# Kernel tuning notes

Measured on AMD Instinct MI355X. Metric: run time of the kernel, lower is better.

Reference implementation:

```python
import jax, jax.numpy as jnp
import numpy as np

CUTOFF = 5.0
NLINKED = 1
CELL_LIST = CUTOFF / NLINKED  # linked-cell edge length
_r = np.arange(-NLINKED, NLINKED + 1)
# torch.cartesian_prod(r1,r1,r1) == meshgrid(indexing='ij') stacked & flattened
LINKED = np.stack(np.meshgrid(_r, _r, _r, indexing='ij'), axis=-1).reshape(1, -1, 3).astype(np.float32)  # (1, 27, 3)


def setup_inputs() -> dict:
    N = 2744
    L = 30.0
    key = jax.random.key(0)
    k1, k2 = jax.random.split(key)
    coordinates = jax.random.uniform(k1, (N, 3), dtype=jnp.float32) * L
    cell = jnp.eye(3, dtype=jnp.float32) * L
    mass = jax.random.uniform(k2, (N,), dtype=jnp.float32) * 15.0 + 1.0
    period_table = jnp.ones((3,), dtype=jnp.int32)  # fully periodic
    return {"period_table": period_table, "coordinates": coordinates, "cell": cell, "mass": mass}


def _forward(period_table, coordinates, cell, mass):
    numatom = coordinates.shape[0]
    # wrap coordinates into the cell relative to atom 0 (fractional coords)
    inv_cell = jnp.linalg.inv(cell)
    inv_coor = coordinates @ inv_cell
    inv_coor = inv_coor - jnp.round(inv_coor - inv_coor[0])
    coordinates = inv_coor @ cell
    # remove center of mass
    com = (mass @ coordinates) / jnp.sum(mass)
    coordinates = coordinates - com[None, :]
    # periodic replicas needed to cover the cutoff
    num_repeats = jnp.ceil(jnp.min(CUTOFF / jnp.abs(cell), axis=0)).astype(jnp.int32)
    num_repeats = period_table.astype(jnp.int32) * num_repeats
    up = num_repeats + 1
    down = -num_repeats
    rs = [jnp.arange(int(down[i]), int(up[i])) for i in range(3)]
    g = jnp.meshgrid(*rs, indexing='ij')
    shifts_frac = jnp.stack(g, axis=-1).reshape(-1, 3).astype(coordinates.dtype)  # (S, 3)
    shifts = shifts_frac @ cell  # (S, 3) cartesian shift vectors
    num_shifts = shifts.shape[0]
    # prod = cartesian_prod(all_shifts, all_atoms).T : row0 shift idx, row1 atom idx
    prod0 = jnp.repeat(jnp.arange(num_shifts), numatom)
    prod1 = jnp.tile(jnp.arange(numatom), num_shifts)
    # shift box so all coords are positive; pad by cutoff
    mincoor = jnp.min(coordinates, axis=0) - CUTOFF - 1e-6
    coordinates = coordinates - mincoor
    maxcoor = jnp.max(coordinates, axis=0) + CUTOFF
    # all periodic images, keep only those inside the padded box
    image = (coordinates[None, :, :] + shifts[:, None, :]).reshape(-1, 3)
    keep = jnp.nonzero(((image < maxcoor) & (image > 0)).all(axis=1))[0]
    image_mask = image[keep]                      # (M, 3)
    prod0 = prod0[keep]
    prod1 = prod1[keep]
    # linked-cell indices
    ori_image_index = jnp.floor(coordinates / CELL_LIST)         # (N, 3)
    neigh_cell = ori_image_index[:, None, :] + jnp.asarray(LINKED)  # (N, 27, 3)
    image_index = jnp.floor(image_mask / CELL_LIST)              # (M, 3)
    max_cell_index = jnp.ceil(maxcoor / CELL_LIST)
    f10 = max_cell_index[1] * max_cell_index[0]
    neigh_cell_index = neigh_cell[:, :, 2] * f10 + neigh_cell[:, :, 1] * max_cell_index[0] + neigh_cell[:, :, 0]  # (N, 27)
    nimage_index = image_index[:, 2] * f10 + image_index[:, 1] * max_cell_index[0] + image_index[:, 0]            # (M,)
    # dense (N, M, 27) cell-index equality -- the memory-bound hot spot
    eq = neigh_cell_index[:, None, :] == nimage_index[None, :, None]
    ai, aj, _ = jnp.nonzero(eq)
    # distance filter on candidate pairs
    d = jnp.linalg.norm(coordinates[ai] - image_mask[aj], axis=-1)
    pair = jnp.nonzero((d < CUTOFF) & (d > 0.001))[0]
    center = ai[pair]
    img = aj[pair]
    shift_idx = prod0[img]
    atom_j = prod1[img]
    neigh_list = jnp.stack([center, atom_j])  # (2, P)
    return neigh_list, shifts[shift_idx], shifts_frac, shift_idx


def reference(period_table, coordinates, cell, mass):
    neigh_list, shifts_out, _, _ = _forward(period_table, coordinates, cell, mass)
    return (neigh_list, shifts_out)
```

## Files before the change

### kernel.cpp

```cpp
#include <hip/hip_runtime.h>
#include <math.h>

#define S_CAP  27
#define MAXNB  128
#define CUT    5.0f
#define NTHR   256
#define GRP    64
#define NMAX   2744



__device__ __forceinline__ void load_cell(const float* __restrict__ cell, float c[3][3])
{
    #pragma unroll
    for (int i = 0; i < 3; i++)
        #pragma unroll
        for (int j = 0; j < 3; j++) c[i][j] = cell[3 * i + j];
}

__device__ __forceinline__ void header_and_shifts(
    const float c[3][3], const int* __restrict__ period,
    const double* __restrict__ pd, const float* __restrict__ pf, int nblkA,
    float* sF, int* sI, float* s_shifts)
{
    #pragma clang fp contract(off)
    int t = threadIdx.x;
    if (t < 64) {
        double SM = 0.0, SX = 0.0, SY = 0.0, SZ = 0.0;
        float MN0 =  __builtin_inff(), MN1 =  __builtin_inff(), MN2 =  __builtin_inff();
        float MX0 = -__builtin_inff(), MX1 = -__builtin_inff(), MX2 = -__builtin_inff();
        for (int b = t; b < nblkA; b += 64) {
            SM += pd[4*b+0]; SX += pd[4*b+1]; SY += pd[4*b+2]; SZ += pd[4*b+3];
            MN0 = fminf(MN0, pf[6*b+0]); MN1 = fminf(MN1, pf[6*b+1]); MN2 = fminf(MN2, pf[6*b+2]);
            MX0 = fmaxf(MX0, pf[6*b+3]); MX1 = fmaxf(MX1, pf[6*b+4]); MX2 = fmaxf(MX2, pf[6*b+5]);
        }
        #pragma unroll
        for (int off = 32; off > 0; off >>= 1) {
            SM += __shfl_down(SM, off, 64);
            SX += __shfl_down(SX, off, 64);
            SY += __shfl_down(SY, off, 64);
            SZ += __shfl_down(SZ, off, 64);
            MN0 = fminf(MN0, __shfl_down(MN0, off, 64));
            MN1 = fminf(MN1, __shfl_down(MN1, off, 64));
            MN2 = fminf(MN2, __shfl_down(MN2, off, 64));
            MX0 = fmaxf(MX0, __shfl_down(MX0, off, 64));
            MX1 = fmaxf(MX1, __shfl_down(MX1, off, 64));
            MX2 = fmaxf(MX2, __shfl_down(MX2, off, 64));
        }
        if (t == 0) {
            float den  = (float)SM;
            float com0 = ((float)SX) / den;
            float com1 = ((float)SY) / den;
            float com2 = ((float)SZ) / den;
            float m20 = ((MN0 - com0) - CUT) - 1e-6f;
            float m21 = ((MN1 - com1) - CUT) - 1e-6f;
            float m22 = ((MN2 - com2) - CUT) - 1e-6f;
            float maxc0 = ((MX0 - com0) - m20) + CUT;
            float maxc1 = ((MX1 - com1) - m21) + CUT;
            float maxc2 = ((MX2 - com2) - m22) + CUT;
            float mcell0 = ceilf(maxc0 / CUT);
            float mcell1 = ceilf(maxc1 / CUT);
            float f10 = mcell1 * mcell0;
            int nr[3];
            for (int j = 0; j < 3; j++) {
                float v = __builtin_inff();
                for (int i = 0; i < 3; i++) {
                    float q = CUT / fabsf(c[i][j]);
                    v = fminf(v, q);
                }
                nr[j] = (int)ceilf(v);
                nr[j] *= period[j];
            }
            int nsz0 = 2*nr[0]+1, nsz1 = 2*nr[1]+1, nsz2 = 2*nr[2]+1;
            int S = nsz0 * nsz1 * nsz2;
            if (S > S_CAP) S = S_CAP;
            sI[0] = S;
            sI[1] = -nr[0]; sI[2] = -nr[1]; sI[3] = -nr[2];
            sI[4] = nsz1;   sI[5] = nsz2;
            sI[6] = (int)mcell0;
            sI[7] = (int)f10;
            sF[0] = maxc0; sF[1] = maxc1; sF[2] = maxc2;
            sF[3] = f10;   sF[4] = mcell0;
            sF[5] = m20;   sF[6] = m21;   sF[7] = m22;
            sF[8] = com0;  sF[9] = com1;  sF[10] = com2;
        }
    }
    __syncthreads();
    int S = sI[0];
    if (t < S) {
        int n1 = sI[4], n2 = sI[5];
        int i0 = t / (n1 * n2);
        int rem = t - i0 * n1 * n2;
        int i1 = rem / n2;
        int i2 = rem - i1 * n2;
        float fx = (float)(sI[1] + i0);
        float fy = (float)(sI[2] + i1);
        float fz = (float)(sI[3] + i2);
        #pragma unroll
        for (int d = 0; d < 3; d++)
            s_shifts[3*t + d] = fx*c[0][d] + fy*c[1][d] + fz*c[2][d];
    }
    __syncthreads();
}

__global__ __launch_bounds__(NTHR)
void kA_wrap(const float* __restrict__ coor, const float* __restrict__ cell,
             const float* __restrict__ mass, float* __restrict__ xv,
             int* __restrict__ sc_agg,
             int* __restrict__ grp_sum, int* __restrict__ grp_arrive,
             double* __restrict__ pd, float* __restrict__ pf, int n, int nagg, int ng)
{
    #pragma clang fp contract(off)
    __shared__ double wsum[4][4];
    __shared__ float  wred[4][6];
    int t    = threadIdx.x;
    int bid  = blockIdx.x;
    int gtid = bid * NTHR + t;
    int lane = t & 63;
    int w    = t >> 6;

    if (gtid < nagg) sc_agg[gtid] = -1;
    if (gtid < ng)   { grp_sum[gtid] = -1; grp_arrive[gtid] = 0; }

    float c[3][3];
    load_cell(cell, c);
    float a00 = c[1][1]*c[2][2] - c[1][2]*c[2][1];
    float a01 = c[0][2]*c[2][1] - c[0][1]*c[2][2];
    float a02 = c[0][1]*c[1][2] - c[0][2]*c[1][1];
    float a10 = c[1][2]*c[2][0] - c[1][0]*c[2][2];
    float a11 = c[0][0]*c[2][2] - c[0][2]*c[2][0];
    float a12 = c[0][2]*c[1][0] - c[0][0]*c[1][2];
    float a20 = c[1][0]*c[2][1] - c[1][1]*c[2][0];
    float a21 = c[0][1]*c[2][0] - c[0][0]*c[2][1];
    float a22 = c[0][0]*c[1][1] - c[0][1]*c[1][0];
    float det = c[0][0]*a00 + c[0][1]*a10 + c[0][2]*a20;
    float inv[3][3] = {{a00/det, a01/det, a02/det},
                       {a10/det, a11/det, a12/det},
                       {a20/det, a21/det, a22/det}};
    float f0[3];
    #pragma unroll
    for (int d = 0; d < 3; d++)
        f0[d] = coor[0]*inv[0][d] + coor[1]*inv[1][d] + coor[2]*inv[2][d];

    double sm = 0.0, sx = 0.0, sy = 0.0, sz = 0.0;
    float mn0 =  __builtin_inff(), mn1 =  __builtin_inff(), mn2 =  __builtin_inff();
    float mx0 = -__builtin_inff(), mx1 = -__builtin_inff(), mx2 = -__builtin_inff();
    if (gtid < n) {
        float p0 = coor[3*gtid], p1 = coor[3*gtid+1], p2 = coor[3*gtid+2];
        float ic[3], ww[3], x[3];
        #pragma unroll
        for (int d = 0; d < 3; d++)
            ic[d] = p0*inv[0][d] + p1*inv[1][d] + p2*inv[2][d];
        #pragma unroll
        for (int d = 0; d < 3; d++)
            ww[d] = ic[d] - rintf(ic[d] - f0[d]);
        #pragma unroll
        for (int d = 0; d < 3; d++)
            x[d] = ww[0]*c[0][d] + ww[1]*c[1][d] + ww[2]*c[2][d];
        xv[3*gtid] = x[0]; xv[3*gtid+1] = x[1]; xv[3*gtid+2] = x[2];
        float m = mass[gtid];
        sm = (double)m;
        sx = (double)m * (double)x[0];
        sy = (double)m * (double)x[1];
        sz = (double)m * (double)x[2];
        mn0 = x[0]; mn1 = x[1]; mn2 = x[2];
        mx0 = x[0]; mx1 = x[1]; mx2 = x[2];
    }
    #pragma unroll
    for (int off = 32; off > 0; off >>= 1) {
        sm += __shfl_down(sm, off, 64);
        sx += __shfl_down(sx, off, 64);
        sy += __shfl_down(sy, off, 64);
        sz += __shfl_down(sz, off, 64);
        mn0 = fminf(mn0, __shfl_down(mn0, off, 64));
        mn1 = fminf(mn1, __shfl_down(mn1, off, 64));
        mn2 = fminf(mn2, __shfl_down(mn2, off, 64));
        mx0 = fmaxf(mx0, __shfl_down(mx0, off, 64));
        mx1 = fmaxf(mx1, __shfl_down(mx1, off, 64));
        mx2 = fmaxf(mx2, __shfl_down(mx2, off, 64));
    }
    if (lane == 0) {
        wsum[w][0] = sm; wsum[w][1] = sx; wsum[w][2] = sy; wsum[w][3] = sz;
        wred[w][0] = mn0; wred[w][1] = mn1; wred[w][2] = mn2;
        wred[w][3] = mx0; wred[w][4] = mx1; wred[w][5] = mx2;
    }
    __syncthreads();
    if (t == 0) {
        double SM = 0.0, SX = 0.0, SY = 0.0, SZ = 0.0;
        float MN0 =  __builtin_inff(), MN1 =  __builtin_inff(), MN2 =  __builtin_inff();
        float MX0 = -__builtin_inff(), MX1 = -__builtin_inff(), MX2 = -__builtin_inff();
        #pragma unroll
        for (int q = 0; q < 4; q++) {
            SM += wsum[q][0]; SX += wsum[q][1]; SY += wsum[q][2]; SZ += wsum[q][3];
            MN0 = fminf(MN0, wred[q][0]); MN1 = fminf(MN1, wred[q][1]); MN2 = fminf(MN2, wred[q][2]);
            MX0 = fmaxf(MX0, wred[q][3]); MX1 = fmaxf(MX1, wred[q][4]); MX2 = fmaxf(MX2, wred[q][5]);
        }
        pd[bid*4+0] = SM; pd[bid*4+1] = SX; pd[bid*4+2] = SY; pd[bid*4+3] = SZ;
        pf[bid*6+0] = MN0; pf[bid*6+1] = MN1; pf[bid*6+2] = MN2;
        pf[bid*6+3] = MX0; pf[bid*6+4] = MX1; pf[bid*6+5] = MX2;
    }
}

__global__ __launch_bounds__(NTHR, 4)
void kC_search_emit(const int* __restrict__ period, const float* __restrict__ cell,
                    const double* __restrict__ pd, const float* __restrict__ pf,
                    const float* __restrict__ xv,
                    int* __restrict__ sc_agg, int* __restrict__ grp_sum,
                    int* __restrict__ grp_arrive,
                    float* __restrict__ out, int nblkA, int nblkC, int n, int P)
{
    #pragma clang fp contract(off)
    __shared__ float sF[12];
    __shared__ int   sI[8];
    __shared__ float s_shifts[3 * S_CAP];
    __shared__ float sux[NMAX], suy[NMAX], suz[NMAX];
    __shared__ int   lst[4][MAXNB];
    __shared__ int   s_np[4];
    __shared__ int   sExcl;
    __shared__ int   sFin;

    const int t    = threadIdx.x;
    const int bid  = blockIdx.x;
    const int lane = t & 63;
    const int w    = t >> 6;
    const int g    = bid / GRP;
    const int gpos = bid - g * GRP;
    const int gbase = g * GRP;
    const int gsz  = min(GRP, nblkC - gbase);

    if (n > NMAX) return;

    float c[3][3];
    load_cell(cell, c);
    header_and_shifts(c, period, pd, pf, nblkA, sF, sI, s_shifts);

    float a00 = c[1][1]*c[2][2] - c[1][2]*c[2][1];
    float a01 = c[0][2]*c[2][1] - c[0][1]*c[2][2];
    float a02 = c[0][1]*c[1][2] - c[0][2]*c[1][1];
    float a10 = c[1][2]*c[2][0] - c[1][0]*c[2][2];
    float a11 = c[0][0]*c[2][2] - c[0][2]*c[2][0];
    float a12 = c[0][2]*c[1][0] - c[0][0]*c[1][2];
    float a20 = c[1][0]*c[2][1] - c[1][1]*c[2][0];
    float a21 = c[0][1]*c[2][0] - c[0][0]*c[2][1];
    float a22 = c[0][0]*c[1][1] - c[0][1]*c[1][0];
    float det = c[0][0]*a00 + c[0][1]*a10 + c[0][2]*a20;
    float inv[3][3] = {{a00/det, a01/det, a02/det},
                       {a10/det, a11/det, a12/det},
                       {a20/det, a21/det, a22/det}};

    {
        const float m20 = sF[5], m21 = sF[6], m22 = sF[7];
        const float com0 = sF[8], com1 = sF[9], com2 = sF[10];
        for (int j = t; j < n; j += NTHR) {
            sux[j] = (xv[3*j]   - com0) - m20;
            suy[j] = (xv[3*j+1] - com1) - m21;
            suz[j] = (xv[3*j+2] - com2) - m22;
        }
    }
    __syncthreads();

    const int atom = bid * 4 + w;
    const bool valid = atom < n;

    {
        int cnt = 0;
        if (valid) {
            const float xi = sux[atom], yi = suy[atom], zi = suz[atom];
            const int d0 = sI[1], d1 = sI[2], d2 = sI[3];
            const int nsz1 = sI[4], nsz2 = sI[5];
            for (int jb = 0; jb < n; jb += 64) {
                int j = jb + lane;
                bool ok = false; int gg = 0;
                if (j < n) {
                    float ujx = sux[j], ujy = suy[j], ujz = suz[j];
                    float dx = xi - ujx, dy = yi - ujy, dz = zi - ujz;
                    float fr0 = rintf(dx*inv[0][0] + dy*inv[1][0] + dz*inv[2][0]);
                    float fr1 = rintf(dx*inv[0][1] + dy*inv[1][1] + dz*inv[2][1]);
                    float fr2 = rintf(dx*inv[0][2] + dy*inv[1][2] + dz*inv[2][2]);
                    float sx = fr0*c[0][0] + fr1*c[1][0] + fr2*c[2][0];
                    float sy = fr0*c[0][1] + fr1*c[1][1] + fr2*c[2][1];
                    float sz = fr0*c[0][2] + fr1*c[1][2] + fr2*c[2][2];
                    float imx = ujx + sx, imy = ujy + sy, imz = ujz + sz;
                    float ddx = xi - imx, ddy = yi - imy, ddz = zi - imz;
                    float ss = ddx*ddx + ddy*ddy + ddz*ddz;
                    float dd = sqrtf(ss);
                    ok = (dd < CUT) && (dd > 0.001f);
                    int i0 = (int)fr0 - d0, i1 = (int)fr1 - d1, i2 = (int)fr2 - d2;
                    int idx = (i0 * nsz1 + i1) * nsz2 + i2;
                    gg = idx * n + j;
                }
                unsigned long long m = __ballot(ok);
                int posn = cnt + (int)__popcll(m & ((1ull << lane) - 1ull));
                if (ok && posn < MAXNB) lst[w][posn] = gg;
                cnt += (int)__popcll(m);
            }
            if (cnt > MAXNB) cnt = MAXNB;
        }
        if (lane == 0) s_np[w] = cnt;
    }
    __syncthreads();

    if (t == 0) {
        int agg = s_np[0] + s_np[1] + s_np[2] + s_np[3];
        __hip_atomic_store(&sc_agg[bid], agg, __ATOMIC_RELAXED, __HIP_MEMORY_SCOPE_AGENT);
        int r = __hip_atomic_fetch_add(&grp_arrive[g], 1, __ATOMIC_ACQ_REL, __HIP_MEMORY_SCOPE_AGENT);
        sFin = (r == gsz - 1) ? 1 : 0;
    }
    __syncthreads();

    if (sFin && w == 0) {
        int idx = gbase + lane;
        int v = 0;
        if (lane < gsz)
            v = __hip_atomic_load(&sc_agg[idx], __ATOMIC_RELAXED, __HIP_MEMORY_SCOPE_AGENT);
        #pragma unroll
        for (int off = 32; off > 0; off >>= 1)
            v += __shfl_down(v, off, 64);
        if (lane == 0)
            __hip_atomic_store(&grp_sum[g], v, __ATOMIC_RELAXED, __HIP_MEMORY_SCOPE_AGENT);
    }

    if (w == 0) {
        int v1 = 0;
        if (lane < g) {
            v1 = __hip_atomic_load(&grp_sum[lane], __ATOMIC_RELAXED, __HIP_MEMORY_SCOPE_AGENT);
            while (v1 == -1) {
                __builtin_amdgcn_s_sleep(2);
                v1 = __hip_atomic_load(&grp_sum[lane], __ATOMIC_RELAXED, __HIP_MEMORY_SCOPE_AGENT);
            }
        }
        int v2 = 0;
        if (lane < gpos) {
            int idx = gbase + lane;
            v2 = __hip_atomic_load(&sc_agg[idx], __ATOMIC_RELAXED, __HIP_MEMORY_SCOPE_AGENT);
            while (v2 == -1) {
                __builtin_amdgcn_s_sleep(2);
                v2 = __hip_atomic_load(&sc_agg[idx], __ATOMIC_RELAXED, __HIP_MEMORY_SCOPE_AGENT);
            }
        }
        int v = v1 + v2;
        #pragma unroll
        for (int off = 32; off > 0; off >>= 1)
            v += __shfl_down(v, off, 64);
        if (lane == 0) sExcl = v;
    }
    __syncthreads();

    if (valid) {
        int cnt = s_np[w];
        int base = sExcl;
        for (int q = 0; q < w; q++) base += s_np[q];
        for (int r = lane; r < cnt; r += 64) {
            int gg = lst[w][r];
            int rank = 0;
            for (int q = 0; q < cnt; q++) rank += (lst[w][q] < gg) ? 1 : 0;
            int p = base + rank;
            if (p < P) {
                int sidx = gg / n;
                int a = gg - sidx * n;
                out[p]     = (float)atom;
                out[P + p] = (float)a;
                out[2*P + 3*p]     = s_shifts[3*sidx];
                out[2*P + 3*p + 1] = s_shifts[3*sidx + 1];
                out[2*P + 3*p + 2] = s_shifts[3*sidx + 2];
            }
        }
    }
}

extern "C" void kernel_launch(void* const* d_in, const int* in_sizes, int n_in,
                              void* d_out, int out_size, void* d_ws, size_t ws_size,
                              hipStream_t stream)
{
    const int*   period = (const int*)d_in[0];
    const float* coor   = (const float*)d_in[1];
    const float* cell   = (const float*)d_in[2];
    const float* mass   = (const float*)d_in[3];
    float* out = (float*)d_out;

    int n = in_sizes[1] / 3;
    int P = out_size / 5;

    char* wp = (char*)d_ws;
    size_t off = 0;
    auto alloc = [&](size_t bytes) -> void* {
        off = (off + 15) & ~(size_t)15;
        void* pp = (void*)(wp + off); off += bytes; return pp;
    };

    int nblkA = (n + NTHR - 1) / NTHR;
    int nblkC = (n + 3) / 4;
    int ng    = (nblkC + GRP - 1) / GRP;

    float*  xv       = (float*) alloc(3 * (size_t)n * 4);
    double* pd       = (double*)alloc((size_t)nblkA * 4 * 8);
    float*  pf       = (float*) alloc((size_t)nblkA * 6 * 4);
    int*    sc_agg   = (int*)   alloc((size_t)nblkC * 4);
    int*    grp_sum  = (int*)   alloc((size_t)ng * 4);
    int*    grp_arr  = (int*)   alloc((size_t)ng * 4);
    (void)ws_size; (void)n_in;

    hipLaunchKernelGGL(kA_wrap, dim3(nblkA), dim3(NTHR), 0, stream,
                       coor, cell, mass, xv, sc_agg, grp_sum, grp_arr,
                       pd, pf, n, nblkC, ng);
    hipLaunchKernelGGL(kC_search_emit, dim3(nblkC), dim3(NTHR), 0, stream,
                       period, cell, pd, pf, xv,
                       sc_agg, grp_sum, grp_arr, out, nblkA, nblkC, n, P);
}
```

Measured before the change: 96.47 us.

## Fuse wrap kernel into search kernel with spin-waited partial reductions

Merges the coordinate-wrapping kernel into the neighbor-search kernel. Each block recomputes all wrapped coordinates straight into shared memory, and the first NSEG blocks also publish per-segment COM and min/max partials. All blocks spin on sentinel values, set by a memset to 0xFF, until those partials are ready. This removes one kernel launch and the global xv round trip, at the cost of redundant per-block wrap work. It adds an inter-block dependency that assumes the producer blocks are resident, and the grp_arrive counter now starts at -1 via memset, which explains the gsz-2 change.

```diff
diff --git a/kernel.cpp b/kernel.cpp
--- a/kernel.cpp
+++ b/kernel.cpp
@@ -7,7 +7,7 @@
 #define NTHR   256
 #define GRP    64
 #define NMAX   2744
-
+#define NSEG   11
 
 
 __device__ __forceinline__ void load_cell(const float* __restrict__ cell, float c[3][3])
@@ -18,21 +18,169 @@
         for (int j = 0; j < 3; j++) c[i][j] = cell[3 * i + j];
 }
 
-__device__ __forceinline__ void header_and_shifts(
-    const float c[3][3], const int* __restrict__ period,
-    const double* __restrict__ pd, const float* __restrict__ pf, int nblkA,
-    float* sF, int* sI, float* s_shifts)
+__global__ __launch_bounds__(NTHR, 4)
+void k_fused(const int* __restrict__ period, const float* __restrict__ coor,
+             const float* __restrict__ cell, const float* __restrict__ mass,
+             double* __restrict__ pd, float* __restrict__ pf,
+             int* __restrict__ sc_agg, int* __restrict__ grp_sum,
+             int* __restrict__ grp_arrive,
+             float* __restrict__ out, int nblkA, int nblkC, int n, int P)
 {
     #pragma clang fp contract(off)
-    int t = threadIdx.x;
+    __shared__ float  sux[NMAX], suy[NMAX], suz[NMAX];
+    __shared__ double wsum[4][4];
+    __shared__ float  wred[4][6];
+    __shared__ float  sF[12];
+    __shared__ int    sI[8];
+    __shared__ float  s_shifts[3 * S_CAP];
+    __shared__ int    lst[4][MAXNB];
+    __shared__ int    s_np[4];
+    __shared__ int    sExcl;
+    __shared__ int    sFin;
+
+    const int t    = threadIdx.x;
+    const int bid  = blockIdx.x;
+    const int lane = t & 63;
+    const int w    = t >> 6;
+    const int g    = bid / GRP;
+    const int gpos = bid - g * GRP;
+    const int gbase = g * GRP;
+    const int gsz  = min(GRP, nblkC - gbase);
+
+    if (n > NMAX) return;
+
+    float c[3][3];
+    load_cell(cell, c);
+    float a00 = c[1][1]*c[2][2] - c[1][2]*c[2][1];
+    float a01 = c[0][2]*c[2][1] - c[0][1]*c[2][2];
+    float a02 = c[0][1]*c[1][2] - c[0][2]*c[1][1];
+    float a10 = c[1][2]*c[2][0] - c[1][0]*c[2][2];
+    float a11 = c[0][0]*c[2][2] - c[0][2]*c[2][0];
+    float a12 = c[0][2]*c[1][0] - c[0][0]*c[1][2];
+    float a20 = c[1][0]*c[2][1] - c[1][1]*c[2][0];
+    float a21 = c[0][1]*c[2][0] - c[0][0]*c[2][1];
+    float a22 = c[0][0]*c[1][1] - c[0][1]*c[1][0];
+    float det = c[0][0]*a00 + c[0][1]*a10 + c[0][2]*a20;
+    float inv[3][3] = {{a00/det, a01/det, a02/det},
+                       {a10/det, a11/det, a12/det},
+                       {a20/det, a21/det, a22/det}};
+    float f0[3];
+    #pragma unroll
+    for (int d = 0; d < 3; d++)
+        f0[d] = coor[0]*inv[0][d] + coor[1]*inv[1][d] + coor[2]*inv[2][d];
+
+    const bool producer = bid < nblkA;
+
+    for (int k = 0; k < NSEG; k++) {
+        int seg = producer ? (k == 0 ? bid : (k <= bid ? k - 1 : k)) : k;
+        int a = seg * NTHR + t;
+        bool va = a < n;
+        float x0 = 0.0f, x1 = 0.0f, x2 = 0.0f;
+        if (va) {
+            float p0 = coor[3*a], p1 = coor[3*a+1], p2 = coor[3*a+2];
+            float ic[3], ww[3];
+            #pragma unroll
+            for (int d = 0; d < 3; d++)
+                ic[d] = p0*inv[0][d] + p1*inv[1][d] + p2*inv[2][d];
+            #pragma unroll
+            for (int d = 0; d < 3; d++)
+                ww[d] = ic[d] - rintf(ic[d] - f0[d]);
+            x0 = ww[0]*c[0][0] + ww[1]*c[1][0] + ww[2]*c[2][0];
+            x1 = ww[0]*c[0][1] + ww[1]*c[1][1] + ww[2]*c[2][1];
+            x2 = ww[0]*c[0][2] + ww[1]*c[1][2] + ww[2]*c[2][2];
+            sux[a] = x0; suy[a] = x1; suz[a] = x2;
+        }
+        if (producer && k == 0) {
+            double sm = 0.0, sx = 0.0, sy = 0.0, sz = 0.0;
+            float mn0 =  __builtin_inff(), mn1 =  __builtin_inff(), mn2 =  __builtin_inff();
+            float mx0 = -__builtin_inff(), mx1 = -__builtin_inff(), mx2 = -__builtin_inff();
+            if (va) {
+                float m = mass[a];
+                sm = (double)m;
+                sx = (double)m * (double)x0;
+                sy = (double)m * (double)x1;
+                sz = (double)m * (double)x2;
+                mn0 = x0; mn1 = x1; mn2 = x2;
+                mx0 = x0; mx1 = x1; mx2 = x2;
+            }
+            #pragma unroll
+            for (int off = 32; off > 0; off >>= 1) {
+                sm += __shfl_down(sm, off, 64);
+                sx += __shfl_down(sx, off, 64);
+                sy += __shfl_down(sy, off, 64);
+                sz += __shfl_down(sz, off, 64);
+                mn0 = fminf(mn0, __shfl_down(mn0, off, 64));
+                mn1 = fminf(mn1, __shfl_down(mn1, off, 64));
+                mn2 = fminf(mn2, __shfl_down(mn2, off, 64));
+                mx0 = fmaxf(mx0, __shfl_down(mx0, off, 64));
+                mx1 = fmaxf(mx1, __shfl_down(mx1, off, 64));
+                mx2 = fmaxf(mx2, __shfl_down(mx2, off, 64));
+            }
+            if (lane == 0) {
+                wsum[w][0] = sm; wsum[w][1] = sx; wsum[w][2] = sy; wsum[w][3] = sz;
+                wred[w][0] = mn0; wred[w][1] = mn1; wred[w][2] = mn2;
+                wred[w][3] = mx0; wred[w][4] = mx1; wred[w][5] = mx2;
+            }
+            __syncthreads();
+            if (t == 0) {
+                double SM = 0.0, SX = 0.0, SY = 0.0, SZ = 0.0;
+                float MN0 =  __builtin_inff(), MN1 =  __builtin_inff(), MN2 =  __builtin_inff();
+                float MX0 = -__builtin_inff(), MX1 = -__builtin_inff(), MX2 = -__builtin_inff();
+                #pragma unroll
+                for (int q = 0; q < 4; q++) {
+                    SM += wsum[q][0]; SX += wsum[q][1]; SY += wsum[q][2]; SZ += wsum[q][3];
+                    MN0 = fminf(MN0, wred[q][0]); MN1 = fminf(MN1, wred[q][1]); MN2 = fminf(MN2, wred[q][2]);
+                    MX0 = fmaxf(MX0, wred[q][3]); MX1 = fmaxf(MX1, wred[q][4]); MX2 = fmaxf(MX2, wred[q][5]);
+                }
+                unsigned long long* pdU = (unsigned long long*)pd;
+                unsigned int*       pfU = (unsigned int*)pf;
+                __hip_atomic_store(&pdU[4*bid+0], __double_as_longlong(SM), __ATOMIC_RELAXED, __HIP_MEMORY_SCOPE_AGENT);
+                __hip_atomic_store(&pdU[4*bid+1], __double_as_longlong(SX), __ATOMIC_RELAXED, __HIP_MEMORY_SCOPE_AGENT);
+                __hip_atomic_store(&pdU[4*bid+2], __double_as_longlong(SY), __ATOMIC_RELAXED, __HIP_MEMORY_SCOPE_AGENT);
+                __hip_atomic_store(&pdU[4*bid+3], __double_as_longlong(SZ), __ATOMIC_RELAXED, __HIP_MEMORY_SCOPE_AGENT);
+                __hip_atomic_store(&pfU[6*bid+0], __float_as_uint(MN0), __ATOMIC_RELAXED, __HIP_MEMORY_SCOPE_AGENT);
+                __hip_atomic_store(&pfU[6*bid+1], __float_as_uint(MN1), __ATOMIC_RELAXED, __HIP_MEMORY_SCOPE_AGENT);
+                __hip_atomic_store(&pfU[6*bid+2], __float_as_uint(MN2), __ATOMIC_RELAXED, __HIP_MEMORY_SCOPE_AGENT);
+                __hip_atomic_store(&pfU[6*bid+3], __float_as_uint(MX0), __ATOMIC_RELAXED, __HIP_MEMORY_SCOPE_AGENT);
+                __hip_atomic_store(&pfU[6*bid+4], __float_as_uint(MX1), __ATOMIC_RELAXED, __HIP_MEMORY_SCOPE_AGENT);
+                __hip_atomic_store(&pfU[6*bid+5], __float_as_uint(MX2), __ATOMIC_RELAXED, __HIP_MEMORY_SCOPE_AGENT);
+            }
+            __syncthreads();
+        }
+    }
+    __syncthreads();
+
     if (t < 64) {
         double SM = 0.0, SX = 0.0, SY = 0.0, SZ = 0.0;
         float MN0 =  __builtin_inff(), MN1 =  __builtin_inff(), MN2 =  __builtin_inff();
         float MX0 = -__builtin_inff(), MX1 = -__builtin_inff(), MX2 = -__builtin_inff();
-        for (int b = t; b < nblkA; b += 64) {
-            SM += pd[4*b+0]; SX += pd[4*b+1]; SY += pd[4*b+2]; SZ += pd[4*b+3];
-            MN0 = fminf(MN0, pf[6*b+0]); MN1 = fminf(MN1, pf[6*b+1]); MN2 = fminf(MN2, pf[6*b+2]);
-            MX0 = fmaxf(MX0, pf[6*b+3]); MX1 = fmaxf(MX1, pf[6*b+4]); MX2 = fmaxf(MX2, pf[6*b+5]);
+        if (lane < nblkA) {
+            const unsigned long long* pdU = (const unsigned long long*)pd;
+            const unsigned int*       pfU = (const unsigned int*)pf;
+            double dv[4]; float fv[6];
+            #pragma unroll
+            for (int i = 0; i < 4; i++) {
+                unsigned long long u;
+                for (;;) {
+                    u = __hip_atomic_load(&pdU[4*lane+i], __ATOMIC_RELAXED, __HIP_MEMORY_SCOPE_AGENT);
+                    if (u != 0xFFFFFFFFFFFFFFFFull) break;
+                    __builtin_amdgcn_s_sleep(2);
+                }
+                dv[i] = __longlong_as_double(u);
+            }
+            #pragma unroll
+            for (int i = 0; i < 6; i++) {
+                unsigned int u;
+                for (;;) {
+                    u = __hip_atomic_load(&pfU[6*lane+i], __ATOMIC_RELAXED, __HIP_MEMORY_SCOPE_AGENT);
+                    if (u != 0xFFFFFFFFu) break;
+                    __builtin_amdgcn_s_sleep(2);
+                }
+                fv[i] = __uint_as_float(u);
+            }
+            SM += dv[0]; SX += dv[1]; SY += dv[2]; SZ += dv[3];
+            MN0 = fminf(MN0, fv[0]); MN1 = fminf(MN1, fv[1]); MN2 = fminf(MN2, fv[2]);
+            MX0 = fmaxf(MX0, fv[3]); MX1 = fmaxf(MX1, fv[4]); MX2 = fmaxf(MX2, fv[5]);
         }
         #pragma unroll
         for (int off = 32; off > 0; off >>= 1) {
@@ -77,8 +225,6 @@
             sI[0] = S;
             sI[1] = -nr[0]; sI[2] = -nr[1]; sI[3] = -nr[2];
             sI[4] = nsz1;   sI[5] = nsz2;
-            sI[6] = (int)mcell0;
-            sI[7] = (int)f10;
             sF[0] = maxc0; sF[1] = maxc1; sF[2] = maxc2;
             sF[3] = f10;   sF[4] = mcell0;
             sF[5] = m20;   sF[6] = m21;   sF[7] = m22;
@@ -86,175 +232,31 @@
         }
     }
     __syncthreads();
-    int S = sI[0];
-    if (t < S) {
-        int n1 = sI[4], n2 = sI[5];
-        int i0 = t / (n1 * n2);
-        int rem = t - i0 * n1 * n2;
-        int i1 = rem / n2;
-        int i2 = rem - i1 * n2;
-        float fx = (float)(sI[1] + i0);
-        float fy = (float)(sI[2] + i1);
-        float fz = (float)(sI[3] + i2);
-        #pragma unroll
-        for (int d = 0; d < 3; d++)
-            s_shifts[3*t + d] = fx*c[0][d] + fy*c[1][d] + fz*c[2][d];
-    }
-    __syncthreads();
-}
-
-__global__ __launch_bounds__(NTHR)
-void kA_wrap(const float* __restrict__ coor, const float* __restrict__ cell,
-             const float* __restrict__ mass, float* __restrict__ xv,
-             int* __restrict__ sc_agg,
-             int* __restrict__ grp_sum, int* __restrict__ grp_arrive,
-             double* __restrict__ pd, float* __restrict__ pf, int n, int nagg, int ng)
-{
-    #pragma clang fp contract(off)
-    __shared__ double wsum[4][4];
-    __shared__ float  wred[4][6];
-    int t    = threadIdx.x;
-    int bid  = blockIdx.x;
-    int gtid = bid * NTHR + t;
-    int lane = t & 63;
-    int w    = t >> 6;
-
-    if (gtid < nagg) sc_agg[gtid] = -1;
-    if (gtid < ng)   { grp_sum[gtid] = -1; grp_arrive[gtid] = 0; }
-
-    float c[3][3];
-    load_cell(cell, c);
-    float a00 = c[1][1]*c[2][2] - c[1][2]*c[2][1];
-    float a01 = c[0][2]*c[2][1] - c[0][1]*c[2][2];
-    float a02 = c[0][1]*c[1][2] - c[0][2]*c[1][1];
-    float a10 = c[1][2]*c[2][0] - c[1][0]*c[2][2];
-    float a11 = c[0][0]*c[2][2] - c[0][2]*c[2][0];
-    float a12 = c[0][2]*c[1][0] - c[0][0]*c[1][2];
-    float a20 = c[1][0]*c[2][1] - c[1][1]*c[2][0];
-    float a21 = c[0][1]*c[2][0] - c[0][0]*c[2][1];
-    float a22 = c[0][0]*c[1][1] - c[0][1]*c[1][0];
-    float det = c[0][0]*a00 + c[0][1]*a10 + c[0][2]*a20;
-    float inv[3][3] = {{a00/det, a01/det, a02/det},
-                       {a10/det, a11/det, a12/det},
-                       {a20/det, a21/det, a22/det}};
-    float f0[3];
-    #pragma unroll
-    for (int d = 0; d < 3; d++)
-        f0[d] = coor[0]*inv[0][d] + coor[1]*inv[1][d] + coor[2]*inv[2][d];
-
-    double sm = 0.0, sx = 0.0, sy = 0.0, sz = 0.0;
-    float mn0 =  __builtin_inff(), mn1 =  __builtin_inff(), mn2 =  __builtin_inff();
-    float mx0 = -__builtin_inff(), mx1 = -__builtin_inff(), mx2 = -__builtin_inff();
-    if (gtid < n) {
-        float p0 = coor[3*gtid], p1 = coor[3*gtid+1], p2 = coor[3*gtid+2];
-        float ic[3], ww[3], x[3];
-        #pragma unroll
-        for (int d = 0; d < 3; d++)
-            ic[d] = p0*inv[0][d] + p1*inv[1][d] + p2*inv[2][d];
-        #pragma unroll
-        for (int d = 0; d < 3; d++)
-            ww[d] = ic[d] - rintf(ic[d] - f0[d]);
-        #pragma unroll
-        for (int d = 0; d < 3; d++)
-            x[d] = ww[0]*c[0][d] + ww[1]*c[1][d] + ww[2]*c[2][d];
-        xv[3*gtid] = x[0]; xv[3*gtid+1] = x[1]; xv[3*gtid+2] = x[2];
-        float m = mass[gtid];
-        sm = (double)m;
-        sx = (double)m * (double)x[0];
-        sy = (double)m * (double)x[1];
-        sz = (double)m * (double)x[2];
-        mn0 = x[0]; mn1 = x[1]; mn2 = x[2];
-        mx0 = x[0]; mx1 = x[1]; mx2 = x[2];
-    }
-    #pragma unroll
-    for (int off = 32; off > 0; off >>= 1) {
-        sm += __shfl_down(sm, off, 64);
-        sx += __shfl_down(sx, off, 64);
-        sy += __shfl_down(sy, off, 64);
-        sz += __shfl_down(sz, off, 64);
-        mn0 = fminf(mn0, __shfl_down(mn0, off, 64));
-        mn1 = fminf(mn1, __shfl_down(mn1, off, 64));
-        mn2 = fminf(mn2, __shfl_down(mn2, off, 64));
-        mx0 = fmaxf(mx0, __shfl_down(mx0, off, 64));
-        mx1 = fmaxf(mx1, __shfl_down(mx1, off, 64));
-        mx2 = fmaxf(mx2, __shfl_down(mx2, off, 64));
-    }
-    if (lane == 0) {
-        wsum[w][0] = sm; wsum[w][1] = sx; wsum[w][2] = sy; wsum[w][3] = sz;
-        wred[w][0] = mn0; wred[w][1] = mn1; wred[w][2] = mn2;
-        wred[w][3] = mx0; wred[w][4] = mx1; wred[w][5] = mx2;
-    }
-    __syncthreads();
-    if (t == 0) {
-        double SM = 0.0, SX = 0.0, SY = 0.0, SZ = 0.0;
-        float MN0 =  __builtin_inff(), MN1 =  __builtin_inff(), MN2 =  __builtin_inff();
-        float MX0 = -__builtin_inff(), MX1 = -__builtin_inff(), MX2 = -__builtin_inff();
-        #pragma unroll
-        for (int q = 0; q < 4; q++) {
-            SM += wsum[q][0]; SX += wsum[q][1]; SY += wsum[q][2]; SZ += wsum[q][3];
-            MN0 = fminf(MN0, wred[q][0]); MN1 = fminf(MN1, wred[q][1]); MN2 = fminf(MN2, wred[q][2]);
-            MX0 = fmaxf(MX0, wred[q][3]); MX1 = fmaxf(MX1, wred[q][4]); MX2 = fmaxf(MX2, wred[q][5]);
-        }
-        pd[bid*4+0] = SM; pd[bid*4+1] = SX; pd[bid*4+2] = SY; pd[bid*4+3] = SZ;
-        pf[bid*6+0] = MN0; pf[bid*6+1] = MN1; pf[bid*6+2] = MN2;
-        pf[bid*6+3] = MX0; pf[bid*6+4] = MX1; pf[bid*6+5] = MX2;
-    }
-}
-
-__global__ __launch_bounds__(NTHR, 4)
-void kC_search_emit(const int* __restrict__ period, const float* __restrict__ cell,
-                    const double* __restrict__ pd, const float* __restrict__ pf,
-                    const float* __restrict__ xv,
-                    int* __restrict__ sc_agg, int* __restrict__ grp_sum,
-                    int* __restrict__ grp_arrive,
-                    float* __restrict__ out, int nblkA, int nblkC, int n, int P)
-{
-    #pragma clang fp contract(off)
-    __shared__ float sF[12];
-    __shared__ int   sI[8];
-    __shared__ float s_shifts[3 * S_CAP];
-    __shared__ float sux[NMAX], suy[NMAX], suz[NMAX];
-    __shared__ int   lst[4][MAXNB];
-    __shared__ int   s_np[4];
-    __shared__ int   sExcl;
-    __shared__ int   sFin;
-
-    const int t    = threadIdx.x;
-    const int bid  = blockIdx.x;
-    const int lane = t & 63;
-    const int w    = t >> 6;
-    const int g    = bid / GRP;
-    const int gpos = bid - g * GRP;
-    const int gbase = g * GRP;
-    const int gsz  = min(GRP, nblkC - gbase);
-
-    if (n > NMAX) return;
-
-    float c[3][3];
-    load_cell(cell, c);
-    header_and_shifts(c, period, pd, pf, nblkA, sF, sI, s_shifts);
-
-    float a00 = c[1][1]*c[2][2] - c[1][2]*c[2][1];
-    float a01 = c[0][2]*c[2][1] - c[0][1]*c[2][2];
-    float a02 = c[0][1]*c[1][2] - c[0][2]*c[1][1];
-    float a10 = c[1][2]*c[2][0] - c[1][0]*c[2][2];
-    float a11 = c[0][0]*c[2][2] - c[0][2]*c[2][0];
-    float a12 = c[0][2]*c[1][0] - c[0][0]*c[1][2];
-    float a20 = c[1][0]*c[2][1] - c[1][1]*c[2][0];
-    float a21 = c[0][1]*c[2][0] - c[0][0]*c[2][1];
-    float a22 = c[0][0]*c[1][1] - c[0][1]*c[1][0];
-    float det = c[0][0]*a00 + c[0][1]*a10 + c[0][2]*a20;
-    float inv[3][3] = {{a00/det, a01/det, a02/det},
-                       {a10/det, a11/det, a12/det},
-                       {a20/det, a21/det, a22/det}};
+    {
+        int S = sI[0];
+        if (t < S) {
+            int n1 = sI[4], n2 = sI[5];
+            int i0 = t / (n1 * n2);
+            int rem = t - i0 * n1 * n2;
+            int i1 = rem / n2;
+            int i2 = rem - i1 * n2;
+            float fx = (float)(sI[1] + i0);
+            float fy = (float)(sI[2] + i1);
+            float fz = (float)(sI[3] + i2);
+            #pragma unroll
+            for (int d = 0; d < 3; d++)
+                s_shifts[3*t + d] = fx*c[0][d] + fy*c[1][d] + fz*c[2][d];
+        }
+    }
+    __syncthreads();
 
     {
         const float m20 = sF[5], m21 = sF[6], m22 = sF[7];
         const float com0 = sF[8], com1 = sF[9], com2 = sF[10];
         for (int j = t; j < n; j += NTHR) {
-            sux[j] = (xv[3*j]   - com0) - m20;
-            suy[j] = (xv[3*j+1] - com1) - m21;
-            suz[j] = (xv[3*j+2] - com2) - m22;
+            sux[j] = (sux[j] - com0) - m20;
+            suy[j] = (suy[j] - com1) - m21;
+            suz[j] = (suz[j] - com2) - m22;
         }
     }
     __syncthreads();
@@ -304,7 +306,7 @@
         int agg = s_np[0] + s_np[1] + s_np[2] + s_np[3];
         __hip_atomic_store(&sc_agg[bid], agg, __ATOMIC_RELAXED, __HIP_MEMORY_SCOPE_AGENT);
         int r = __hip_atomic_fetch_add(&grp_arrive[g], 1, __ATOMIC_ACQ_REL, __HIP_MEMORY_SCOPE_AGENT);
-        sFin = (r == gsz - 1) ? 1 : 0;
+        sFin = (r == gsz - 2) ? 1 : 0;
     }
     __syncthreads();
 
@@ -388,22 +390,22 @@
         void* pp = (void*)(wp + off); off += bytes; return pp;
     };
 
-    int nblkA = (n + NTHR - 1) / NTHR;
+    int nblkA = NSEG;
     int nblkC = (n + 3) / 4;
     int ng    = (nblkC + GRP - 1) / GRP;
 
-    float*  xv       = (float*) alloc(3 * (size_t)n * 4);
+    size_t sent_beg = (off + 15) & ~(size_t)15;
     double* pd       = (double*)alloc((size_t)nblkA * 4 * 8);
     float*  pf       = (float*) alloc((size_t)nblkA * 6 * 4);
-    int*    sc_agg   = (int*)   alloc((size_t)nblkC * 4);
+    int*    sc_agg   = (int*)   alloc((size_t)(ng * GRP) * 4);
     int*    grp_sum  = (int*)   alloc((size_t)ng * 4);
     int*    grp_arr  = (int*)   alloc((size_t)ng * 4);
+    size_t sent_end = off;
     (void)ws_size; (void)n_in;
 
-    hipLaunchKernelGGL(kA_wrap, dim3(nblkA), dim3(NTHR), 0, stream,
-                       coor, cell, mass, xv, sc_agg, grp_sum, grp_arr,
-                       pd, pf, n, nblkC, ng);
-    hipLaunchKernelGGL(kC_search_emit, dim3(nblkC), dim3(NTHR), 0, stream,
-                       period, cell, pd, pf, xv,
+    hipMemsetAsync(wp + sent_beg, 0xFF, sent_end - sent_beg, stream);
+
+    hipLaunchKernelGGL(k_fused, dim3(nblkC), dim3(NTHR), 0, stream,
+                       period, coor, cell, mass, pd, pf,
                        sc_agg, grp_sum, grp_arr, out, nblkA, nblkC, n, P);
 }
```

Measured after the change: 112.2 us. +16.3%, slower.

## Split per-atom search across two waves and add cheap minimum-image prefilter

Applied to the files above, without the earlier changes.

Each atom's candidate scan is now split between two wavefronts (512-thread blocks), each covering half of the atoms. A cheap orthorhombic minimum-image squared-distance prefilter compacts candidates into a shared queue, and the full image/shift computation with sqrt runs only on the survivors. Ranking for ordered output now merges counts across the two half-lists. The aim is to cut per-pair ALU work and raise parallelism, at the cost of more LDS, a larger block, and possible dropped candidates if the queue overflows CAPQ.

```diff
diff --git a/kernel.cpp b/kernel.cpp
--- a/kernel.cpp
+++ b/kernel.cpp
@@ -1,13 +1,14 @@
 #include <hip/hip_runtime.h>
 #include <math.h>
 
-#define S_CAP  27
-#define MAXNB  128
-#define CUT    5.0f
-#define NTHR   256
-#define GRP    64
-#define NMAX   2744
-
+#define S_CAP   27
+#define MAXNB   128
+#define CAPQ    128
+#define CUT     5.0f
+#define NTHR    256
+#define NTHC    512
+#define GRP     64
+#define NMAX    2744
 
 
 __device__ __forceinline__ void load_cell(const float* __restrict__ cell, float c[3][3])
@@ -77,8 +78,6 @@
             sI[0] = S;
             sI[1] = -nr[0]; sI[2] = -nr[1]; sI[3] = -nr[2];
             sI[4] = nsz1;   sI[5] = nsz2;
-            sI[6] = (int)mcell0;
-            sI[7] = (int)f10;
             sF[0] = maxc0; sF[1] = maxc1; sF[2] = maxc2;
             sF[3] = f10;   sF[4] = mcell0;
             sF[5] = m20;   sF[6] = m21;   sF[7] = m22;
@@ -201,7 +200,7 @@
     }
 }
 
-__global__ __launch_bounds__(NTHR, 4)
+__global__ __launch_bounds__(NTHC, 6)
 void kC_search_emit(const int* __restrict__ period, const float* __restrict__ cell,
                     const double* __restrict__ pd, const float* __restrict__ pf,
                     const float* __restrict__ xv,
@@ -214,8 +213,9 @@
     __shared__ int   sI[8];
     __shared__ float s_shifts[3 * S_CAP];
     __shared__ float sux[NMAX], suy[NMAX], suz[NMAX];
-    __shared__ int   lst[4][MAXNB];
-    __shared__ int   s_np[4];
+    __shared__ int   que[8][CAPQ];
+    __shared__ int   lst[8][MAXNB];
+    __shared__ int   s_np[8];
     __shared__ int   sExcl;
     __shared__ int   sFin;
 
@@ -248,10 +248,16 @@
                        {a10/det, a11/det, a12/det},
                        {a20/det, a21/det, a22/det}};
 
+    const bool diag = (c[0][1]==0.0f) && (c[0][2]==0.0f) && (c[1][0]==0.0f) &&
+                      (c[1][2]==0.0f) && (c[2][0]==0.0f) && (c[2][1]==0.0f);
+    const float L0 = c[0][0], L1 = c[1][1], L2 = c[2][2];
+    const float iL0 = inv[0][0], iL1 = inv[1][1], iL2 = inv[2][2];
+    const float PRETH = CUT*CUT + 0.02f;
+
     {
         const float m20 = sF[5], m21 = sF[6], m22 = sF[7];
         const float com0 = sF[8], com1 = sF[9], com2 = sF[10];
-        for (int j = t; j < n; j += NTHR) {
+        for (int j = t; j < n; j += NTHC) {
             sux[j] = (xv[3*j]   - com0) - m20;
             suy[j] = (xv[3*j+1] - com1) - m21;
             suz[j] = (xv[3*j+2] - com2) - m22;
@@ -259,49 +265,85 @@
     }
     __syncthreads();
 
-    const int atom = bid * 4 + w;
+    const int atom = bid * 4 + (w >> 1);
+    const int half = w & 1;
     const bool valid = atom < n;
 
-    {
-        int cnt = 0;
-        if (valid) {
-            const float xi = sux[atom], yi = suy[atom], zi = suz[atom];
-            const int d0 = sI[1], d1 = sI[2], d2 = sI[3];
-            const int nsz1 = sI[4], nsz2 = sI[5];
-            for (int jb = 0; jb < n; jb += 64) {
-                int j = jb + lane;
-                bool ok = false; int gg = 0;
-                if (j < n) {
-                    float ujx = sux[j], ujy = suy[j], ujz = suz[j];
-                    float dx = xi - ujx, dy = yi - ujy, dz = zi - ujz;
+    int cnt = 0;
+    if (valid) {
+        const float xi = sux[atom], yi = suy[atom], zi = suz[atom];
+        const int nh = (n + 1) >> 1;
+        const int jlo = half * nh;
+        const int jhi = min(n, jlo + nh);
+
+        int qcnt = 0;
+        for (int jb = jlo; jb < jhi; jb += 64) {
+            int j = jb + lane;
+            bool pre = false;
+            if (j < jhi) {
+                float dx = xi - sux[j], dy = yi - suy[j], dz = zi - suz[j];
+                float ssp;
+                if (diag) {
+                    float f0r = dx - L0 * rintf(dx * iL0);
+                    float f1r = dy - L1 * rintf(dy * iL1);
+                    float f2r = dz - L2 * rintf(dz * iL2);
+                    ssp = f0r*f0r + f1r*f1r + f2r*f2r;
+                } else {
                     float fr0 = rintf(dx*inv[0][0] + dy*inv[1][0] + dz*inv[2][0]);
                     float fr1 = rintf(dx*inv[0][1] + dy*inv[1][1] + dz*inv[2][1]);
                     float fr2 = rintf(dx*inv[0][2] + dy*inv[1][2] + dz*inv[2][2]);
-                    float sx = fr0*c[0][0] + fr1*c[1][0] + fr2*c[2][0];
-                    float sy = fr0*c[0][1] + fr1*c[1][1] + fr2*c[2][1];
-                    float sz = fr0*c[0][2] + fr1*c[1][2] + fr2*c[2][2];
-                    float imx = ujx + sx, imy = ujy + sy, imz = ujz + sz;
-                    float ddx = xi - imx, ddy = yi - imy, ddz = zi - imz;
-                    float ss = ddx*ddx + ddy*ddy + ddz*ddz;
-                    float dd = sqrtf(ss);
-                    ok = (dd < CUT) && (dd > 0.001f);
-                    int i0 = (int)fr0 - d0, i1 = (int)fr1 - d1, i2 = (int)fr2 - d2;
-                    int idx = (i0 * nsz1 + i1) * nsz2 + i2;
-                    gg = idx * n + j;
+                    float ddx = dx - (fr0*c[0][0] + fr1*c[1][0] + fr2*c[2][0]);
+                    float ddy = dy - (fr0*c[0][1] + fr1*c[1][1] + fr2*c[2][1]);
+                    float ddz = dz - (fr0*c[0][2] + fr1*c[1][2] + fr2*c[2][2]);
+                    ssp = ddx*ddx + ddy*ddy + ddz*ddz;
                 }
-                unsigned long long m = __ballot(ok);
-                int posn = cnt + (int)__popcll(m & ((1ull << lane) - 1ull));
-                if (ok && posn < MAXNB) lst[w][posn] = gg;
-                cnt += (int)__popcll(m);
-            }
-            if (cnt > MAXNB) cnt = MAXNB;
-        }
-        if (lane == 0) s_np[w] = cnt;
-    }
+                pre = ssp < PRETH;
+            }
+            unsigned long long m = __ballot(pre);
+            int posn = qcnt + (int)__popcll(m & ((1ull << lane) - 1ull));
+            if (pre && posn < CAPQ) que[w][posn] = j;
+            qcnt += (int)__popcll(m);
+        }
+        if (qcnt > CAPQ) qcnt = CAPQ;
+
+        const int d0 = sI[1], d1 = sI[2], d2 = sI[3];
+        const int nsz1 = sI[4], nsz2 = sI[5];
+        for (int qb = 0; qb < qcnt; qb += 64) {
+            int r = qb + lane;
+            bool ok = false; int gg = 0;
+            if (r < qcnt) {
+                int j = que[w][r];
+                float ujx = sux[j], ujy = suy[j], ujz = suz[j];
+                float dx = xi - ujx, dy = yi - ujy, dz = zi - ujz;
+                float fr0 = rintf(dx*inv[0][0] + dy*inv[1][0] + dz*inv[2][0]);
+                float fr1 = rintf(dx*inv[0][1] + dy*inv[1][1] + dz*inv[2][1]);
+                float fr2 = rintf(dx*inv[0][2] + dy*inv[1][2] + dz*inv[2][2]);
+                float sx = fr0*c[0][0] + fr1*c[1][0] + fr2*c[2][0];
+                float sy = fr0*c[0][1] + fr1*c[1][1] + fr2*c[2][1];
+                float sz = fr0*c[0][2] + fr1*c[1][2] + fr2*c[2][2];
+                float imx = ujx + sx, imy = ujy + sy, imz = ujz + sz;
+                float ddx = xi - imx, ddy = yi - imy, ddz = zi - imz;
+                float ss = ddx*ddx + ddy*ddy + ddz*ddz;
+                float dd = sqrtf(ss);
+                ok = (dd < CUT) && (dd > 0.001f);
+                int i0 = (int)fr0 - d0, i1 = (int)fr1 - d1, i2 = (int)fr2 - d2;
+                int idx = (i0 * nsz1 + i1) * nsz2 + i2;
+                gg = idx * n + j;
+            }
+            unsigned long long m = __ballot(ok);
+            int posn = cnt + (int)__popcll(m & ((1ull << lane) - 1ull));
+            if (ok && posn < MAXNB) lst[w][posn] = gg;
+            cnt += (int)__popcll(m);
+        }
+        if (cnt > MAXNB) cnt = MAXNB;
+    }
+    if (lane == 0) s_np[w] = cnt;
     __syncthreads();
 
     if (t == 0) {
-        int agg = s_np[0] + s_np[1] + s_np[2] + s_np[3];
+        int agg = 0;
+        #pragma unroll
+        for (int q = 0; q < 8; q++) agg += s_np[q];
         __hip_atomic_store(&sc_agg[bid], agg, __ATOMIC_RELAXED, __HIP_MEMORY_SCOPE_AGENT);
         int r = __hip_atomic_fetch_add(&grp_arrive[g], 1, __ATOMIC_ACQ_REL, __HIP_MEMORY_SCOPE_AGENT);
         sFin = (r == gsz - 1) ? 1 : 0;
@@ -346,14 +388,16 @@
     }
     __syncthreads();
 
-    if (valid) {
-        int cnt = s_np[w];
+    if (valid && cnt > 0) {
+        const int wa = w & ~1, wb = wa | 1;
+        const int cA = s_np[wa], cB = s_np[wb];
         int base = sExcl;
-        for (int q = 0; q < w; q++) base += s_np[q];
+        for (int q = 0; q < wa; q++) base += s_np[q];
         for (int r = lane; r < cnt; r += 64) {
             int gg = lst[w][r];
             int rank = 0;
-            for (int q = 0; q < cnt; q++) rank += (lst[w][q] < gg) ? 1 : 0;
+            for (int q = 0; q < cA; q++) rank += (lst[wa][q] < gg) ? 1 : 0;
+            for (int q = 0; q < cB; q++) rank += (lst[wb][q] < gg) ? 1 : 0;
             int p = base + rank;
             if (p < P) {
                 int sidx = gg / n;
@@ -403,7 +447,7 @@
     hipLaunchKernelGGL(kA_wrap, dim3(nblkA), dim3(NTHR), 0, stream,
                        coor, cell, mass, xv, sc_agg, grp_sum, grp_arr,
                        pd, pf, n, nblkC, ng);
-    hipLaunchKernelGGL(kC_search_emit, dim3(nblkC), dim3(NTHR), 0, stream,
+    hipLaunchKernelGGL(kC_search_emit, dim3(nblkC), dim3(NTHC), 0, stream,
                        period, cell, pd, pf, xv,
                        sc_agg, grp_sum, grp_arr, out, nblkA, nblkC, n, P);
 }
```

New measurement: 90.06 us. 6.6% less time.
